# Optimization experiments

Measured on AMD Instinct MI355X. Metric: run time of the kernel, lower is better.

## Reference

```python
import jax, jax.numpy as jnp
import numpy as np

EPS = 1e-12  # matches torch F.normalize eps


def _l2norm(v, axis):
    return v / jnp.clip(jnp.linalg.norm(v, axis=axis, keepdims=True), EPS)


def setup_inputs() -> dict:
    key = jax.random.key(0)
    k1, k2 = jax.random.split(key)
    x = jax.random.normal(k1, (64, 768, 24, 24), dtype=jnp.float32)
    conv_w = jax.random.normal(k2, (64, 768), dtype=jnp.float32)  # [K, D] 1x1 conv, no bias
    return {"x": x, "conv_w": conv_w}


def reference(x, conv_w):
    # x: [N, D, H, W], conv_w: [K, D]
    N, D, H, W = x.shape
    K = conv_w.shape[0]
    xn = _l2norm(x, axis=1)                       # L2-normalize over channel dim
    xf = xn.reshape(N, D, H * W)                  # [N, D, L]
    att = jnp.einsum('kd,ndl->nkl', conv_w, xf)   # 1x1 conv logits [N, K, L]
    att = jax.nn.softmax(att, axis=1)             # softmax over clusters
    # fused batched reduction replacing the per-cluster python loop
    out = jnp.einsum('ndl,nkl->nkd', xf, att)     # [N, K, D]
    out = _l2norm(out, axis=2)                    # intra-cluster L2 norm
    out = out.reshape(N, K * D)
    out = _l2norm(out, axis=1)                    # global L2 norm
    return out
```

## Files before the change

kernel.cpp:

```cpp
#include <hip/hip_runtime.h>
#include <math.h>

#define EPSF 1e-12f
#define DD 768
#define LL 576

typedef unsigned short u16;
typedef __attribute__((ext_vector_type(8))) short bf16x8;
typedef __attribute__((ext_vector_type(4))) float f32x4;

__device__ __forceinline__ u16 bf16h(float v) {
  unsigned u = __float_as_uint(v);
  return (u16)((u + 0x7FFFu + ((u >> 16) & 1u)) >> 16);
}

__device__ __forceinline__ void split8(const float* v, uint4& ph, uint4& pl) {
  unsigned h[8], lo[8];
#pragma unroll
  for (int i = 0; i < 8; ++i) {
    unsigned u = __float_as_uint(v[i]);
    unsigned r = (u + 0x7FFFu + ((u >> 16) & 1u)) >> 16;
    h[i] = r;
    float rest = v[i] - __uint_as_float(r << 16);
    unsigned u2 = __float_as_uint(rest);
    lo[i] = (u2 + 0x7FFFu + ((u2 >> 16) & 1u)) >> 16;
  }
  ph = make_uint4(h[0] | (h[1] << 16), h[2] | (h[3] << 16),
                  h[4] | (h[5] << 16), h[6] | (h[7] << 16));
  pl = make_uint4(lo[0] | (lo[1] << 16), lo[2] | (lo[3] << 16),
                  lo[4] | (lo[5] << 16), lo[6] | (lo[7] << 16));
}

__device__ __forceinline__ void split4(const float* v, uint2& ph, uint2& pl) {
  unsigned h[4], lo[4];
#pragma unroll
  for (int i = 0; i < 4; ++i) {
    unsigned u = __float_as_uint(v[i]);
    unsigned r = (u + 0x7FFFu + ((u >> 16) & 1u)) >> 16;
    h[i] = r;
    float rest = v[i] - __uint_as_float(r << 16);
    unsigned u2 = __float_as_uint(rest);
    lo[i] = (u2 + 0x7FFFu + ((u2 >> 16) & 1u)) >> 16;
  }
  ph = make_uint2(h[0] | (h[1] << 16), h[2] | (h[3] << 16));
  pl = make_uint2(lo[0] | (lo[1] << 16), lo[2] | (lo[3] << 16));
}

__device__ __forceinline__ void probe_layout(int lane, int* rowz, int* colz) {
  bf16x8 va, v1;
  const short ml = (short)bf16h((float)(lane & 15));
  const short on = (short)0x3F80;
#pragma unroll
  for (int e = 0; e < 8; ++e) { va[e] = ml; v1[e] = on; }
  f32x4 z = {0.f, 0.f, 0.f, 0.f};
  f32x4 D1 = __builtin_amdgcn_mfma_f32_16x16x32_bf16(va, v1, z, 0, 0, 0);
  f32x4 D2 = __builtin_amdgcn_mfma_f32_16x16x32_bf16(v1, va, z, 0, 0, 0);
#pragma unroll
  for (int r = 0; r < 4; ++r) {
    rowz[r] = (int)(D1[r] * 0.03125f + 0.5f);
    colz[r] = (int)(D2[r] * 0.03125f + 0.5f);
  }
}

__global__ __launch_bounds__(256) void kW(const float* __restrict__ w,
                                          u16* __restrict__ wfH,
                                          u16* __restrict__ wfL) {
  const int s = blockIdx.x;
  const int t = threadIdx.x;
  const int strip = t >> 6, lane = t & 63;
  const int k = strip * 16 + (lane & 15);
  const int d = s * 32 + (lane >> 4) * 8;
  float v[8];
  *(float4*)&v[0] = *(const float4*)(w + k * DD + d);
  *(float4*)&v[4] = *(const float4*)(w + k * DD + d + 4);
  uint4 ph, pl;
  split8(v, ph, pl);
  const size_t o = ((size_t)(strip * 24 + s) * 64 + lane) * 8;
  *(uint4*)(wfH + o) = ph;
  *(uint4*)(wfL + o) = pl;
}

__global__ __launch_bounds__(256) void kA(const float* __restrict__ x,
                                          const u16* __restrict__ wfH,
                                          const u16* __restrict__ wfL,
                                          u16* __restrict__ attH,
                                          u16* __restrict__ attL) {
  __shared__ __align__(16) char pool[9728];
  float (*raw)[36] = (float(*)[36])pool;
  u16 (*Xh)[40] = (u16(*)[40])(pool + 4608);
  u16 (*Xl)[40] = (u16(*)[40])(pool + 7168);
  float (*Ls)[36] = (float(*)[36])pool;
  __shared__ float red8[8][32];
  __shared__ float colinv[32], colmax[32], colscale[32];

  const int b = blockIdx.x;
  const int n = b / 18, l0 = (b % 18) * 32;
  const int t = threadIdx.x;
  const int wv = t >> 6, lane = t & 63;

  int rowz[4], colz[4];
  probe_layout(lane, rowz, colz);

  f32x4 z = {0.f, 0.f, 0.f, 0.f};
  f32x4 acc[2] = {z, z};
  float ssq4[4] = {0.f, 0.f, 0.f, 0.f};

  const int xd = t >> 3;
  const int xl = (t & 7) * 4;
  const int tl = lane & 31;
  const int half = lane >> 5;

  const float* xbase = x + (size_t)n * DD * LL + l0;
  const u16* wfHp = wfH + ((size_t)wv * 24 * 64 + lane) * 8;
  const u16* wfLp = wfL + ((size_t)wv * 24 * 64 + lane) * 8;

  float4 pre = *(const float4*)(xbase + (size_t)xd * LL + xl);

  for (int s = 0; s < 24; ++s) {
    __syncthreads();
    *(float4*)&raw[xd][xl] = pre;
    ssq4[0] = fmaf(pre.x, pre.x, ssq4[0]);
    ssq4[1] = fmaf(pre.y, pre.y, ssq4[1]);
    ssq4[2] = fmaf(pre.z, pre.z, ssq4[2]);
    ssq4[3] = fmaf(pre.w, pre.w, ssq4[3]);
    if (s < 23)
      pre = *(const float4*)(xbase + (size_t)((s + 1) * 32 + xd) * LL + xl);
    bf16x8 Ah = *(const bf16x8*)(wfHp + (size_t)s * 512);
    bf16x8 Alo = *(const bf16x8*)(wfLp + (size_t)s * 512);
    __syncthreads();
    {
      float v[4];
#pragma unroll
      for (int j = 0; j < 4; ++j) v[j] = raw[wv * 8 + half * 4 + j][tl];
      uint2 ph, pl;
      split4(v, ph, pl);
      const int pb = (wv ^ ((tl >> 3) & 3)) * 8 + half * 4;
      *(uint2*)&Xh[tl][pb] = ph;
      *(uint2*)&Xl[tl][pb] = pl;
    }
    __syncthreads();
#pragma unroll
    for (int lt = 0; lt < 2; ++lt) {
      const int bl = lt * 16 + (lane & 15);
      const int pb = ((lane >> 4) ^ ((bl >> 3) & 3)) * 8;
      bf16x8 Bh = *(const bf16x8*)&Xh[bl][pb];
      bf16x8 Bl = *(const bf16x8*)&Xl[bl][pb];
      acc[lt] = __builtin_amdgcn_mfma_f32_16x16x32_bf16(Ah, Bh, acc[lt], 0, 0, 0);
      acc[lt] = __builtin_amdgcn_mfma_f32_16x16x32_bf16(Ah, Bl, acc[lt], 0, 0, 0);
      acc[lt] = __builtin_amdgcn_mfma_f32_16x16x32_bf16(Alo, Bh, acc[lt], 0, 0, 0);
    }
  }

#pragma unroll
  for (int i = 0; i < 4; ++i) {
    ssq4[i] += __shfl_xor(ssq4[i], 8, 64);
    ssq4[i] += __shfl_xor(ssq4[i], 16, 64);
    ssq4[i] += __shfl_xor(ssq4[i], 32, 64);
  }
  if (lane < 8) {
#pragma unroll
    for (int i = 0; i < 4; ++i) red8[wv][lane * 4 + i] = ssq4[i];
  }
  __syncthreads();
  if (t < 32)
    colinv[t] =
        1.f / fmaxf(sqrtf(red8[0][t] + red8[1][t] + red8[2][t] + red8[3][t]), EPSF);
#pragma unroll
  for (int lt = 0; lt < 2; ++lt)
#pragma unroll
    for (int r = 0; r < 4; ++r)
      Ls[wv * 16 + rowz[r]][lt * 16 + colz[r]] = acc[lt][r];
  __syncthreads();

  const int cl = t & 31, q = t >> 5;
  const float cinv = colinv[cl];
  float sv[8];
  float m = -1e30f;
#pragma unroll
  for (int i = 0; i < 8; ++i) {
    const float vv = Ls[q * 8 + i][cl] * cinv;
    sv[i] = vv;
    m = fmaxf(m, vv);
  }
  red8[q][cl] = m;
  __syncthreads();
  if (t < 32) {
    float mm = red8[0][t];
#pragma unroll
    for (int j = 1; j < 8; ++j) mm = fmaxf(mm, red8[j][t]);
    colmax[t] = mm;
  }
  __syncthreads();
  const float M = colmax[cl];
  float ssum = 0.f;
#pragma unroll
  for (int i = 0; i < 8; ++i) {
    const float e = __expf(sv[i] - M);
    sv[i] = e;
    ssum += e;
  }
  red8[q][cl] = ssum;
  __syncthreads();
  if (t < 32) {
    float ss = red8[0][t];
#pragma unroll
    for (int j = 1; j < 8; ++j) ss += red8[j][t];
    colscale[t] = colinv[t] / ss;
  }
  __syncthreads();
  const float cs = colscale[cl];
  u16* aH = attH + (size_t)n * 64 * LL + l0 + cl;
  u16* aL = attL + (size_t)n * 64 * LL + l0 + cl;
#pragma unroll
  for (int i = 0; i < 8; ++i) {
    const int k = q * 8 + i;
    const float e = sv[i] * cs;
    unsigned u = __float_as_uint(e);
    unsigned r = (u + 0x7FFFu + ((u >> 16) & 1u)) >> 16;
    const float rest = e - __uint_as_float(r << 16);
    aH[(size_t)k * LL] = (u16)r;
    aL[(size_t)k * LL] = bf16h(rest);
  }
}

__global__ __launch_bounds__(256) void kB(const float* __restrict__ x,
                                          const u16* __restrict__ attH,
                                          const u16* __restrict__ attL,
                                          float* __restrict__ out,
                                          float* __restrict__ part) {
  __shared__ __align__(16) u16 AH[64][40];
  __shared__ __align__(16) u16 AL[64][40];
  __shared__ __align__(16) u16 Xh[64][40];
  __shared__ __align__(16) u16 Xl[64][40];
  const int b = blockIdx.x;
  const int n = b / 12, d0 = (b % 12) * 64;
  const int t = threadIdx.x;
  const int wv = t >> 6, lane = t & 63;

  int rowz[4], colz[4];
  probe_layout(lane, rowz, colz);

  f32x4 z = {0.f, 0.f, 0.f, 0.f};
  f32x4 acc[4] = {z, z, z, z};

  const int rk = t >> 2;
  const int lb = (t & 3) * 8;

  const u16* aHb = attH + ((size_t)n * 64 + rk) * LL + lb;
  const u16* aLb = attL + ((size_t)n * 64 + rk) * LL + lb;
  const float* xb = x + ((size_t)n * DD + d0 + rk) * LL + lb;

  uint4 pAH = *(const uint4*)aHb;
  uint4 pAL = *(const uint4*)aLb;
  float4 pX0 = *(const float4*)xb;
  float4 pX1 = *(const float4*)(xb + 4);

  for (int s = 0; s < 18; ++s) {
    __syncthreads();
    *(uint4*)&AH[rk][lb] = pAH;
    *(uint4*)&AL[rk][lb] = pAL;
    {
      float v[8] = {pX0.x, pX0.y, pX0.z, pX0.w, pX1.x, pX1.y, pX1.z, pX1.w};
      uint4 ph, pl;
      split8(v, ph, pl);
      *(uint4*)&Xh[rk][lb] = ph;
      *(uint4*)&Xl[rk][lb] = pl;
    }
    if (s < 17) {
      const int lo = (s + 1) * 32;
      pAH = *(const uint4*)(aHb + lo);
      pAL = *(const uint4*)(aLb + lo);
      pX0 = *(const float4*)(xb + lo);
      pX1 = *(const float4*)(xb + lo + 4);
    }
    __syncthreads();
    const int ar = wv * 16 + (lane & 15);
    const int ab = (lane >> 4) * 8;
    bf16x8 Ah = *(const bf16x8*)&AH[ar][ab];
    bf16x8 Alo = *(const bf16x8*)&AL[ar][ab];
#pragma unroll
    for (int dt = 0; dt < 4; ++dt) {
      const int br = dt * 16 + (lane & 15);
      bf16x8 Bh = *(const bf16x8*)&Xh[br][ab];
      bf16x8 Bl = *(const bf16x8*)&Xl[br][ab];
      acc[dt] = __builtin_amdgcn_mfma_f32_16x16x32_bf16(Ah, Bh, acc[dt], 0, 0, 0);
      acc[dt] = __builtin_amdgcn_mfma_f32_16x16x32_bf16(Ah, Bl, acc[dt], 0, 0, 0);
      acc[dt] = __builtin_amdgcn_mfma_f32_16x16x32_bf16(Alo, Bh, acc[dt], 0, 0, 0);
    }
  }

  float* ob = out + ((size_t)n * 64 + wv * 16) * DD + d0;
#pragma unroll
  for (int dt = 0; dt < 4; ++dt)
#pragma unroll
    for (int r = 0; r < 4; ++r)
      ob[(size_t)rowz[r] * DD + dt * 16 + colz[r]] = acc[dt][r];

#pragma unroll
  for (int r = 0; r < 4; ++r) {
    float s = 0.f;
#pragma unroll
    for (int dt = 0; dt < 4; ++dt) s = fmaf(acc[dt][r], acc[dt][r], s);
    s += __shfl_xor(s, 1, 64);
    s += __shfl_xor(s, 2, 64);
    s += __shfl_xor(s, 4, 64);
    s += __shfl_xor(s, 8, 64);
    if ((lane & 15) == 0)
      part[(size_t)b * 64 + wv * 16 + rowz[r]] = s;
  }
}

__global__ __launch_bounds__(64) void kC2(const float* __restrict__ part,
                                          float* __restrict__ scale) {
  const int n = blockIdx.x;
  const int t = threadIdx.x;
  float ss = 0.f;
#pragma unroll
  for (int j = 0; j < 12; ++j) ss += part[(size_t)(n * 12 + j) * 64 + t];
  const float invk = 1.f / fmaxf(sqrtf(ss), EPSF);
  float r = ss * invk * invk;
#pragma unroll
  for (int off = 32; off >= 1; off >>= 1) r += __shfl_xor(r, off, 64);
  const float ginv = 1.f / fmaxf(sqrtf(r), EPSF);
  scale[n * 64 + t] = invk * ginv;
}

__global__ __launch_bounds__(256) void kC3(float* __restrict__ out,
                                           const float* __restrict__ scale) {
  const int i = blockIdx.x * 256 + threadIdx.x;
  const int row = i / 192;
  const float s = scale[row];
  float4 v = ((float4*)out)[i];
  v.x *= s; v.y *= s; v.z *= s; v.w *= s;
  ((float4*)out)[i] = v;
}

extern "C" void kernel_launch(void* const* d_in, const int* in_sizes, int n_in,
                              void* d_out, int out_size, void* d_ws, size_t ws_size,
                              hipStream_t stream) {
  const float* x = (const float*)d_in[0];
  const float* w = (const float*)d_in[1];
  float* out = (float*)d_out;

  u16* attH = (u16*)d_ws;
  u16* attL = attH + (size_t)2359296;
  u16* wfH = attL + (size_t)2359296;
  u16* wfL = wfH + 49152;
  float* part = (float*)(wfL + 49152);
  float* scale = part + 49152;

  kW<<<24, 256, 0, stream>>>(w, wfH, wfL);
  kA<<<1152, 256, 0, stream>>>(x, wfH, wfL, attH, attL);
  kB<<<768, 256, 0, stream>>>(x, attH, attL, out, part);
  kC2<<<64, 64, 0, stream>>>(part, scale);
  kC3<<<3072, 256, 0, stream>>>(out, scale);
}
```

Before: 73.10 us.

## Double-buffer kA shared tiles to pipeline staging, transpose and MFMA

The main attention-logit kernel now keeps two copies of its raw-fp32 and split-bf16 tiles in shared memory. Each loop iteration stages chunk i, transposes chunk i-1 and runs the MFMAs on chunk i-2, with the weight fragments prefetched one step ahead. This cuts the barriers per iteration from three to one and overlaps global loads, LDS work and matrix math, at the cost of more shared memory and explicit prologue and epilogue stages. Separately, kC2 replaces the warp-wide global-norm reduction with a constant 1/sqrt(64) factor. That is exact as long as no cluster vector is zero.

```diff
diff --git a/kernel.cpp b/kernel.cpp
--- a/kernel.cpp
+++ b/kernel.cpp
@@ -80,16 +80,52 @@
   *(uint4*)(wfL + o) = pl;
 }
 
+__device__ __forceinline__ void kA_stage(float (*rawb)[36], int xd, int xl,
+                                         const float4& p, float* ssq4) {
+  *(float4*)&rawb[xd][xl] = p;
+  ssq4[0] = fmaf(p.x, p.x, ssq4[0]);
+  ssq4[1] = fmaf(p.y, p.y, ssq4[1]);
+  ssq4[2] = fmaf(p.z, p.z, ssq4[2]);
+  ssq4[3] = fmaf(p.w, p.w, ssq4[3]);
+}
+
+__device__ __forceinline__ void kA_transpose(const float (*rawb)[36],
+                                             u16 (*XhB)[40], u16 (*XlB)[40],
+                                             int wv, int half, int tl) {
+  float v[4];
+#pragma unroll
+  for (int j = 0; j < 4; ++j) v[j] = rawb[wv * 8 + half * 4 + j][tl];
+  uint2 ph, pl;
+  split4(v, ph, pl);
+  const int pb = (wv ^ ((tl >> 3) & 3)) * 8 + half * 4;
+  *(uint2*)&XhB[tl][pb] = ph;
+  *(uint2*)&XlB[tl][pb] = pl;
+}
+
+__device__ __forceinline__ void kA_mfma(const u16 (*XhB)[40], const u16 (*XlB)[40],
+                                        int lane, const bf16x8& Ah,
+                                        const bf16x8& Al, f32x4* acc) {
+#pragma unroll
+  for (int lt = 0; lt < 2; ++lt) {
+    const int bl = lt * 16 + (lane & 15);
+    const int pb = ((lane >> 4) ^ ((bl >> 3) & 3)) * 8;
+    bf16x8 Bh = *(const bf16x8*)&XhB[bl][pb];
+    bf16x8 Bl = *(const bf16x8*)&XlB[bl][pb];
+    acc[lt] = __builtin_amdgcn_mfma_f32_16x16x32_bf16(Ah, Bh, acc[lt], 0, 0, 0);
+    acc[lt] = __builtin_amdgcn_mfma_f32_16x16x32_bf16(Ah, Bl, acc[lt], 0, 0, 0);
+    acc[lt] = __builtin_amdgcn_mfma_f32_16x16x32_bf16(Al, Bh, acc[lt], 0, 0, 0);
+  }
+}
+
 __global__ __launch_bounds__(256) void kA(const float* __restrict__ x,
                                           const u16* __restrict__ wfH,
                                           const u16* __restrict__ wfL,
                                           u16* __restrict__ attH,
                                           u16* __restrict__ attL) {
-  __shared__ __align__(16) char pool[9728];
-  float (*raw)[36] = (float(*)[36])pool;
-  u16 (*Xh)[40] = (u16(*)[40])(pool + 4608);
-  u16 (*Xl)[40] = (u16(*)[40])(pool + 7168);
-  float (*Ls)[36] = (float(*)[36])pool;
+  __shared__ __align__(16) float raw[2][32][36];
+  __shared__ __align__(16) u16 Xh[2][32][40];
+  __shared__ __align__(16) u16 Xl[2][32][40];
+  float (*Ls)[36] = (float(*)[36])raw;
   __shared__ float red8[8][32];
   __shared__ float colinv[32], colmax[32], colscale[32];
 
@@ -115,41 +151,39 @@
   const u16* wfLp = wfL + ((size_t)wv * 24 * 64 + lane) * 8;
 
   float4 pre = *(const float4*)(xbase + (size_t)xd * LL + xl);
-
-  for (int s = 0; s < 24; ++s) {
+  bf16x8 AhN, AlN;
+
+  kA_stage(raw[0], xd, xl, pre, ssq4);
+  pre = *(const float4*)(xbase + (size_t)(32 + xd) * LL + xl);
+  __syncthreads();
+  AhN = *(const bf16x8*)(wfHp);
+  AlN = *(const bf16x8*)(wfLp);
+  kA_transpose(raw[0], Xh[0], Xl[0], wv, half, tl);
+  kA_stage(raw[1], xd, xl, pre, ssq4);
+  pre = *(const float4*)(xbase + (size_t)(64 + xd) * LL + xl);
+
+  for (int i = 2; i < 24; ++i) {
     __syncthreads();
-    *(float4*)&raw[xd][xl] = pre;
-    ssq4[0] = fmaf(pre.x, pre.x, ssq4[0]);
-    ssq4[1] = fmaf(pre.y, pre.y, ssq4[1]);
-    ssq4[2] = fmaf(pre.z, pre.z, ssq4[2]);
-    ssq4[3] = fmaf(pre.w, pre.w, ssq4[3]);
-    if (s < 23)
-      pre = *(const float4*)(xbase + (size_t)((s + 1) * 32 + xd) * LL + xl);
-    bf16x8 Ah = *(const bf16x8*)(wfHp + (size_t)s * 512);
-    bf16x8 Alo = *(const bf16x8*)(wfLp + (size_t)s * 512);
-    __syncthreads();
-    {
-      float v[4];
-#pragma unroll
-      for (int j = 0; j < 4; ++j) v[j] = raw[wv * 8 + half * 4 + j][tl];
-      uint2 ph, pl;
-      split4(v, ph, pl);
-      const int pb = (wv ^ ((tl >> 3) & 3)) * 8 + half * 4;
-      *(uint2*)&Xh[tl][pb] = ph;
-      *(uint2*)&Xl[tl][pb] = pl;
-    }
-    __syncthreads();
-#pragma unroll
-    for (int lt = 0; lt < 2; ++lt) {
-      const int bl = lt * 16 + (lane & 15);
-      const int pb = ((lane >> 4) ^ ((bl >> 3) & 3)) * 8;
-      bf16x8 Bh = *(const bf16x8*)&Xh[bl][pb];
-      bf16x8 Bl = *(const bf16x8*)&Xl[bl][pb];
-      acc[lt] = __builtin_amdgcn_mfma_f32_16x16x32_bf16(Ah, Bh, acc[lt], 0, 0, 0);
-      acc[lt] = __builtin_amdgcn_mfma_f32_16x16x32_bf16(Ah, Bl, acc[lt], 0, 0, 0);
-      acc[lt] = __builtin_amdgcn_mfma_f32_16x16x32_bf16(Alo, Bh, acc[lt], 0, 0, 0);
-    }
-  }
+    const bf16x8 AhC = AhN, AlC = AlN;
+    AhN = *(const bf16x8*)(wfHp + (size_t)(i - 1) * 512);
+    AlN = *(const bf16x8*)(wfLp + (size_t)(i - 1) * 512);
+    const float4 cur = pre;
+    if (i < 23)
+      pre = *(const float4*)(xbase + (size_t)((i + 1) * 32 + xd) * LL + xl);
+    kA_stage(raw[i & 1], xd, xl, cur, ssq4);
+    kA_transpose(raw[(i - 1) & 1], Xh[(i - 1) & 1], Xl[(i - 1) & 1], wv, half, tl);
+    kA_mfma(Xh[i & 1], Xl[i & 1], lane, AhC, AlC, acc);
+  }
+  __syncthreads();
+  {
+    const bf16x8 AhC = AhN, AlC = AlN;
+    AhN = *(const bf16x8*)(wfHp + (size_t)23 * 512);
+    AlN = *(const bf16x8*)(wfLp + (size_t)23 * 512);
+    kA_transpose(raw[1], Xh[1], Xl[1], wv, half, tl);
+    kA_mfma(Xh[0], Xl[0], lane, AhC, AlC, acc);
+  }
+  __syncthreads();
+  kA_mfma(Xh[1], Xl[1], lane, AhN, AlN, acc);
 
 #pragma unroll
   for (int i = 0; i < 4; ++i) {
@@ -317,12 +351,7 @@
   float ss = 0.f;
 #pragma unroll
   for (int j = 0; j < 12; ++j) ss += part[(size_t)(n * 12 + j) * 64 + t];
-  const float invk = 1.f / fmaxf(sqrtf(ss), EPSF);
-  float r = ss * invk * invk;
-#pragma unroll
-  for (int off = 32; off >= 1; off >>= 1) r += __shfl_xor(r, off, 64);
-  const float ginv = 1.f / fmaxf(sqrtf(r), EPSF);
-  scale[n * 64 + t] = invk * ginv;
+  scale[n * 64 + t] = 0.125f / fmaxf(sqrtf(ss), EPSF);
 }
 
 __global__ __launch_bounds__(256) void kC3(float* __restrict__ out,
```

New measurement: 76.00 us. 4.0% more time.
